# Performance work log

Hardware: AMD Instinct MI355X
Metric: run time of the kernel (lower is better)

Reference implementation:

```python
import jax, jax.numpy as jnp
import numpy as np

B, T, DIM, H, KV, HD = 1, 2048, 2048, 16, 4, 128


def _rope_tables(T, hd):
    half = hd // 2
    inv_freq = 1.0 / (10000.0 ** (np.arange(0, half, dtype=np.float32) / half))
    t = np.arange(T, dtype=np.float32)
    freqs = np.outer(t, inv_freq)                # [T, hd/2]
    emb = np.concatenate([freqs, freqs], axis=-1)  # [T, hd]
    return jnp.asarray(np.cos(emb)), jnp.asarray(np.sin(emb))


def setup_inputs() -> dict:
    key = jax.random.key(0)
    kx, kq, kk, kv, ko = jax.random.split(key, 5)
    s = 0.02
    x = jax.random.normal(kx, (B, T, DIM), dtype=jnp.float32)
    wq = jax.random.normal(kq, (H * HD, DIM), dtype=jnp.float32) * s
    wk = jax.random.normal(kk, (KV * HD, DIM), dtype=jnp.float32) * s
    wv = jax.random.normal(kv, (KV * HD, DIM), dtype=jnp.float32) * s
    wo = jax.random.normal(ko, (DIM, H * HD), dtype=jnp.float32) * s
    cos, sin = _rope_tables(T, HD)
    return {"x": x, "wq": wq, "wk": wk, "wv": wv, "wo": wo, "cos": cos, "sin": sin}


def _rotate_half(u):
    u1, u2 = jnp.split(u, 2, axis=-1)
    return jnp.concatenate([-u2, u1], axis=-1)


def _apply_rope(u, cos, sin):
    # u: [B, T, h, hd]; cos/sin: [T, hd]
    c = cos[None, :, None, :]
    s = sin[None, :, None, :]
    return u * c + _rotate_half(u) * s


def reference(x, wq, wk, wv, wo, cos, sin):
    b, t, dim = x.shape
    hd = cos.shape[1]
    h = wq.shape[0] // hd
    kvh = wk.shape[0] // hd
    rep = h // kvh
    scale = hd ** -0.5

    q = (x @ wq.T).reshape(b, t, h, hd)
    k = (x @ wk.T).reshape(b, t, kvh, hd)
    v = (x @ wv.T).reshape(b, t, kvh, hd)

    q = _apply_rope(q, cos, sin)
    k = _apply_rope(k, cos, sin)

    # Group queries by shared KV head instead of materializing repeat_kv
    qg = q.reshape(b, t, kvh, rep, hd)
    scores = jnp.einsum('bqgrd,bkgd->bgrqk', qg, k) * scale  # [b,g,r,T,T]
    causal = jnp.tril(jnp.ones((t, t), dtype=bool))
    scores = jnp.where(causal[None, None, None], scores, jnp.float32(-1e30))
    attn = jax.nn.softmax(scores, axis=-1)
    out = jnp.einsum('bgrqk,bkgd->bqgrd', attn, v).reshape(b, t, h * hd)
    return out @ wo.T
```

## Files before the change

### kernel.cpp

```cpp
#include <hip/hip_runtime.h>
#include <hip/hip_bf16.h>

typedef unsigned short u16;
typedef __attribute__((ext_vector_type(8))) short bf16x8;
typedef __attribute__((ext_vector_type(4))) float f32x4;

#define T_SEQ 2048
#define DIM   2048
#define NH    16
#define NKV   4
#define HD    128
#define NQKV  3072
#define SCALE 0.08838834764831845f
#define CHUNK 512

__device__ __forceinline__ u16 f2bf(float f) {
  unsigned int u = __float_as_uint(f);
  unsigned int r = (u + 0x7fffu + ((u >> 16) & 1u)) >> 16;
  return (u16)r;
}
__device__ __forceinline__ float bf2f(u16 v) {
  return __uint_as_float(((unsigned int)v) << 16);
}

#define B1 1048576
#define B2 2097152
#define B3 2359296
#define B4 2621440
#define B5 3670016
__global__ void cast_all(const float4* __restrict__ x,  const float4* __restrict__ wq,
                         const float4* __restrict__ wk, const float4* __restrict__ wv,
                         const float4* __restrict__ wo,
                         ushort4* __restrict__ xb, ushort4* __restrict__ wqkvb,
                         ushort4* __restrict__ wob) {
  int i = blockIdx.x * 256 + threadIdx.x;
  const float4* src; ushort4* dst; int j;
  if (i < B1)      { src = x;  dst = xb;               j = i; }
  else if (i < B2) { src = wq; dst = wqkvb;            j = i - B1; }
  else if (i < B3) { src = wk; dst = wqkvb + 1048576;  j = i - B2; }
  else if (i < B4) { src = wv; dst = wqkvb + 1310720;  j = i - B3; }
  else             { src = wo; dst = wob;              j = i - B4; }
  float4 v = src[j];
  ushort4 o;
  o.x = f2bf(v.x); o.y = f2bf(v.y); o.z = f2bf(v.z); o.w = f2bf(v.w);
  dst[j] = o;
}

#define BM 128
#define BN 128
#define BK 64
#define LDP 72

__global__ __launch_bounds__(256) void gemm_bt(
    const u16* __restrict__ A, const u16* __restrict__ W,
    float* __restrict__ Cf, u16* __restrict__ Cb, int M, int N, int K)
{
  __shared__ u16 As[BM * LDP];
  __shared__ u16 Bs[BN * LDP];
  const int tid  = threadIdx.x;
  const int lane = tid & 63;
  const int wave = tid >> 6;
  const int ln   = lane & 15;
  const int quad = lane >> 4;
  const int m0 = blockIdx.y * BM;
  const int n0 = blockIdx.x * BN;
  const int wm = (wave >> 1) * 64;
  const int wn = (wave & 1) * 64;

  const int sr = tid >> 3;
  const int sc = (tid & 7) * 8;

  f32x4 acc[4][4] = {};

  for (int k0 = 0; k0 < K; k0 += BK) {
#pragma unroll
    for (int c = 0; c < 4; ++c) {
      int row = c * 32 + sr;
      *(bf16x8*)&As[row * LDP + sc] =
          *(const bf16x8*)&A[(size_t)(m0 + row) * K + k0 + sc];
      *(bf16x8*)&Bs[row * LDP + sc] =
          *(const bf16x8*)&W[(size_t)(n0 + row) * K + k0 + sc];
    }
    __syncthreads();
#pragma unroll
    for (int ks = 0; ks < 2; ++ks) {
      bf16x8 af[4], bfr[4];
#pragma unroll
      for (int mt = 0; mt < 4; ++mt)
        af[mt] = *(const bf16x8*)&As[(wm + mt * 16 + ln) * LDP + ks * 32 + quad * 8];
#pragma unroll
      for (int nt = 0; nt < 4; ++nt)
        bfr[nt] = *(const bf16x8*)&Bs[(wn + nt * 16 + ln) * LDP + ks * 32 + quad * 8];
#pragma unroll
      for (int mt = 0; mt < 4; ++mt)
#pragma unroll
        for (int nt = 0; nt < 4; ++nt)
          acc[mt][nt] = __builtin_amdgcn_mfma_f32_16x16x32_bf16(
              af[mt], bfr[nt], acc[mt][nt], 0, 0, 0);
    }
    __syncthreads();
  }

#pragma unroll
  for (int mt = 0; mt < 4; ++mt)
#pragma unroll
    for (int nt = 0; nt < 4; ++nt)
#pragma unroll
      for (int r = 0; r < 4; ++r) {
        int row = m0 + wm + mt * 16 + quad * 4 + r;
        int col = n0 + wn + nt * 16 + ln;
        if (Cb) Cb[(size_t)row * N + col] = f2bf(acc[mt][nt][r]);
        else    Cf[(size_t)row * N + col] = acc[mt][nt][r];
      }
}

__global__ void rope_fused(const u16* __restrict__ QKVb,
                           const float* __restrict__ cosT,
                           const float* __restrict__ sinT,
                           u16* __restrict__ Qs, u16* __restrict__ Kb,
                           u16* __restrict__ Vt)
{
  int b = blockIdx.x, d = threadIdx.x;
  if (b < T_SEQ * NH) {
    int t = b >> 4;
    int h = b & 15;
    const u16* row = QKVb + (size_t)t * NQKV + h * HD;
    float u = bf2f(row[d]);
    float pr = (d < 64) ? -bf2f(row[d + 64]) : bf2f(row[d - 64]);
    float c = cosT[t * HD + d], s = sinT[t * HD + d];
    Qs[(size_t)b * HD + d] = f2bf((u * c + pr * s) * SCALE);
  } else if (b < T_SEQ * (NH + NKV)) {
    int b2 = b - T_SEQ * NH;
    int t = b2 >> 2;
    int g = b2 & 3;
    const u16* row = QKVb + (size_t)t * NQKV + DIM + g * HD;
    float u = bf2f(row[d]);
    float pr = (d < 64) ? -bf2f(row[d + 64]) : bf2f(row[d - 64]);
    float c = cosT[t * HD + d], s = sinT[t * HD + d];
    Kb[((size_t)g * T_SEQ + t) * HD + d] = f2bf(u * c + pr * s);
  } else {
    int b3 = b - T_SEQ * (NH + NKV);
    int idx = b3 * 128 + d;
    int t  = idx & (T_SEQ - 1);
    int dd = (idx >> 11) & (HD - 1);
    int g  = idx >> 18;
    Vt[idx] = QKVb[(size_t)t * NQKV + DIM + NKV * HD + g * HD + dd];
  }
}

#define KSP 136
#define VSP 72
#define PSP 72
__global__ __launch_bounds__(256) void flash_partial(
    const u16* __restrict__ Qs, const u16* __restrict__ Kb,
    const u16* __restrict__ Vt, u16* __restrict__ Opart,
    float* __restrict__ lpart)
{
  const int c  = blockIdx.x;
  const int qi = blockIdx.y;
  const int h  = blockIdx.z;
  const int b  = qi >> 2;
  if (c > b) return;
  const int g  = h >> 2;
  const int q0 = qi << 7;
  const int k0 = c << 9;
  const int kend = min(k0 + CHUNK, q0 + 128);

  __shared__ u16 Ks[64 * KSP];
  __shared__ u16 Vs[HD * VSP];
  __shared__ u16 Ps[4][32 * PSP];

  const int tid  = threadIdx.x;
  const int lane = tid & 63;
  const int w    = tid >> 6;
  const int ln   = lane & 15;
  const int quad = lane >> 4;

  bf16x8 aq[2][4];
#pragma unroll
  for (int mt = 0; mt < 2; ++mt) {
    const u16* qp = Qs + ((size_t)(q0 + w * 32 + mt * 16 + ln) * NH + h) * HD + quad * 8;
#pragma unroll
    for (int ks = 0; ks < 4; ++ks) aq[mt][ks] = *(const bf16x8*)&qp[ks * 32];
  }

  f32x4 o[2][8] = {};
  float rs[2][4] = {};

  const int rb0 = q0 + w * 32 + quad * 4;
  const int rb1 = rb0 + 16;
  const int rmax0 = q0 + w * 32 + 15;
  const int rmax1 = q0 + w * 32 + 31;

  const u16* kbase = Kb + (size_t)g * T_SEQ * HD;

  for (int jb = k0; jb < kend; jb += 64) {
    {
      int r = tid >> 4, cc = (tid & 15) * 8;
#pragma unroll
      for (int i = 0; i < 4; ++i) {
        int row = i * 16 + r;
        *(bf16x8*)&Ks[row * KSP + cc] =
            *(const bf16x8*)&kbase[(size_t)(jb + row) * HD + cc];
      }
    }
    {
      int r = tid >> 3, cc = (tid & 7) * 8;
#pragma unroll
      for (int i = 0; i < 4; ++i) {
        int row = i * 32 + r;
        *(bf16x8*)&Vs[row * VSP + cc] =
            *(const bf16x8*)&Vt[(size_t)(g * HD + row) * T_SEQ + jb + cc];
      }
    }
    __syncthreads();

    if (jb <= rmax1) {
      const bool do0  = (jb <= rmax0);
      const bool diag = (jb >= q0);

#pragma unroll
      for (int nb = 0; nb < 4; ++nb) {
        bf16x8 kf[4];
#pragma unroll
        for (int ks = 0; ks < 4; ++ks)
          kf[ks] = *(const bf16x8*)&Ks[(nb * 16 + ln) * KSP + ks * 32 + quad * 8];
        f32x4 s0 = {}, s1 = {};
#pragma unroll
        for (int ks = 0; ks < 4; ++ks) {
          if (do0) s0 = __builtin_amdgcn_mfma_f32_16x16x32_bf16(aq[0][ks], kf[ks], s0, 0, 0, 0);
          s1 = __builtin_amdgcn_mfma_f32_16x16x32_bf16(aq[1][ks], kf[ks], s1, 0, 0, 0);
        }
        const int j = jb + nb * 16 + ln;
#pragma unroll
        for (int r = 0; r < 4; ++r) {
          if (do0) {
            float p = (!diag || j <= rb0 + r) ? __expf(s0[r]) : 0.f;
            rs[0][r] += p;
            Ps[w][(quad * 4 + r) * PSP + nb * 16 + ln] = f2bf(p);
          }
          float p1 = (!diag || j <= rb1 + r) ? __expf(s1[r]) : 0.f;
          rs[1][r] += p1;
          Ps[w][(16 + quad * 4 + r) * PSP + nb * 16 + ln] = f2bf(p1);
        }
      }

#pragma unroll
      for (int kst = 0; kst < 2; ++kst) {
        bf16x8 ap0, ap1;
        if (do0) ap0 = *(const bf16x8*)&Ps[w][ln * PSP + kst * 32 + quad * 8];
        ap1 = *(const bf16x8*)&Ps[w][(16 + ln) * PSP + kst * 32 + quad * 8];
#pragma unroll
        for (int nb8 = 0; nb8 < 8; ++nb8) {
          bf16x8 bv = *(const bf16x8*)&Vs[(nb8 * 16 + ln) * VSP + kst * 32 + quad * 8];
          if (do0) o[0][nb8] = __builtin_amdgcn_mfma_f32_16x16x32_bf16(ap0, bv, o[0][nb8], 0, 0, 0);
          o[1][nb8] = __builtin_amdgcn_mfma_f32_16x16x32_bf16(ap1, bv, o[1][nb8], 0, 0, 0);
        }
      }
    }
    __syncthreads();
  }

  const int slot = h * 40 + 2 * b * (b + 1) + (qi & 3) * (b + 1) + c;
  u16*   op = Opart + (size_t)slot * (128 * 128);
  float* lp = lpart + (size_t)slot * 128;
#pragma unroll
  for (int mt = 0; mt < 2; ++mt) {
#pragma unroll
    for (int r = 0; r < 4; ++r)
#pragma unroll
      for (int off = 1; off < 16; off <<= 1)
        rs[mt][r] += __shfl_xor(rs[mt][r], off);
    int rowb = w * 32 + mt * 16 + quad * 4;
#pragma unroll
    for (int r = 0; r < 4; ++r) {
#pragma unroll
      for (int nb8 = 0; nb8 < 8; ++nb8)
        op[(rowb + r) * 128 + nb8 * 16 + ln] = f2bf(o[mt][nb8][r]);
      if (ln == 0) lp[rowb + r] = rs[mt][r];
    }
  }
}

__global__ void flash_reduce(const u16* __restrict__ Opart,
                             const float* __restrict__ lpart,
                             u16* __restrict__ AO)
{
  const int h = blockIdx.y;
  const int d = threadIdx.x & 127;
  const int t = blockIdx.x * 2 + (threadIdx.x >> 7);
  const int qi = t >> 7, r = t & 127;
  const int b = qi >> 2;
  const int base = h * 40 + 2 * b * (b + 1) + (qi & 3) * (b + 1);
  float so = 0.f, sl = 0.f;
  for (int cc = 0; cc <= b; ++cc) {
    so += bf2f(Opart[(size_t)(base + cc) * (128 * 128) + r * 128 + d]);
    sl += lpart[(size_t)(base + cc) * 128 + r];
  }
  AO[(size_t)t * DIM + h * HD + d] = f2bf(so / sl);
}

extern "C" void kernel_launch(void* const* d_in, const int* in_sizes, int n_in,
                              void* d_out, int out_size, void* d_ws, size_t ws_size,
                              hipStream_t stream) {
  const float* x    = (const float*)d_in[0];
  const float* wq   = (const float*)d_in[1];
  const float* wk   = (const float*)d_in[2];
  const float* wv   = (const float*)d_in[3];
  const float* wo   = (const float*)d_in[4];
  const float* cosT = (const float*)d_in[5];
  const float* sinT = (const float*)d_in[6];
  float* out = (float*)d_out;

  char* ws = (char*)d_ws;
  const size_t MB = 1024 * 1024;
  u16*   xb    = (u16*)(ws + 0 * MB);
  u16*   wqkvb = (u16*)(ws + 8 * MB);
  u16*   wob   = (u16*)(ws + 20 * MB);
  u16*   QKVb  = (u16*)(ws + 28 * MB);
  u16*   Qs    = (u16*)(ws + 8 * MB);
  u16*   Kb    = (u16*)(ws + 16 * MB);
  u16*   Vt    = (u16*)(ws + 18 * MB);
  u16*   AO    = (u16*)(ws + 0 * MB);
  u16*   Opart = (u16*)(ws + 28 * MB);
  float* lpart = (float*)(ws + 48 * MB);

  cast_all<<<B5 / 256, 256, 0, stream>>>(
      (const float4*)x, (const float4*)wq, (const float4*)wk, (const float4*)wv,
      (const float4*)wo, (ushort4*)xb, (ushort4*)wqkvb, (ushort4*)wob);

  gemm_bt<<<dim3(NQKV / BN, T_SEQ / BM), 256, 0, stream>>>(
      xb, wqkvb, nullptr, QKVb, T_SEQ, NQKV, DIM);

  rope_fused<<<T_SEQ * (NH + NKV) + (NKV * HD * T_SEQ) / 128, HD, 0, stream>>>(
      QKVb, cosT, sinT, Qs, Kb, Vt);

  flash_partial<<<dim3(4, 16, 16), 256, 0, stream>>>(Qs, Kb, Vt, Opart, lpart);
  flash_reduce<<<dim3(T_SEQ / 2, NH), 256, 0, stream>>>(Opart, lpart, AO);

  gemm_bt<<<dim3(DIM / BN, T_SEQ / BM), 256, 0, stream>>>(
      AO, wob, out, nullptr, T_SEQ, DIM, DIM);
}
```

Baseline: 284.6 us.

## Process two query heads per flash block to reuse shared K/V tiles

Each flash_partial block now handles two query heads of the same KV group instead of one, halving the grid's z dimension. K and V tiles loaded into shared memory are reused across both heads, halving global K/V traffic and load/sync overhead per unit of work. The cost is doubled accumulator and Q-fragment registers (o becomes 2x2x8 f32x4) plus a larger P buffer in LDS, which may reduce occupancy or cause spills, and fewer blocks are launched.

```diff
diff --git a/kernel.cpp b/kernel.cpp
--- a/kernel.cpp
+++ b/kernel.cpp
@@ -158,17 +158,18 @@
 {
   const int c  = blockIdx.x;
   const int qi = blockIdx.y;
-  const int h  = blockIdx.z;
+  const int hp = blockIdx.z;
   const int b  = qi >> 2;
   if (c > b) return;
-  const int g  = h >> 2;
+  const int g  = hp >> 1;
+  const int h0 = g * 4 + (hp & 1) * 2;
   const int q0 = qi << 7;
   const int k0 = c << 9;
   const int kend = min(k0 + CHUNK, q0 + 128);
 
   __shared__ u16 Ks[64 * KSP];
   __shared__ u16 Vs[HD * VSP];
-  __shared__ u16 Ps[4][32 * PSP];
+  __shared__ u16 Ps[4][64 * PSP];
 
   const int tid  = threadIdx.x;
   const int lane = tid & 63;
@@ -176,16 +177,18 @@
   const int ln   = lane & 15;
   const int quad = lane >> 4;
 
-  bf16x8 aq[2][4];
-#pragma unroll
-  for (int mt = 0; mt < 2; ++mt) {
-    const u16* qp = Qs + ((size_t)(q0 + w * 32 + mt * 16 + ln) * NH + h) * HD + quad * 8;
-#pragma unroll
-    for (int ks = 0; ks < 4; ++ks) aq[mt][ks] = *(const bf16x8*)&qp[ks * 32];
-  }
-
-  f32x4 o[2][8] = {};
-  float rs[2][4] = {};
+  bf16x8 aq[2][2][4];
+#pragma unroll
+  for (int hh = 0; hh < 2; ++hh)
+#pragma unroll
+    for (int mt = 0; mt < 2; ++mt) {
+      const u16* qp = Qs + ((size_t)(q0 + w * 32 + mt * 16 + ln) * NH + h0 + hh) * HD + quad * 8;
+#pragma unroll
+      for (int ks = 0; ks < 4; ++ks) aq[hh][mt][ks] = *(const bf16x8*)&qp[ks * 32];
+    }
+
+  f32x4 o[2][2][8] = {};
+  float rs[2][2][4] = {};
 
   const int rb0 = q0 + w * 32 + quad * 4;
   const int rb1 = rb0 + 16;
@@ -225,59 +228,72 @@
 #pragma unroll
         for (int ks = 0; ks < 4; ++ks)
           kf[ks] = *(const bf16x8*)&Ks[(nb * 16 + ln) * KSP + ks * 32 + quad * 8];
-        f32x4 s0 = {}, s1 = {};
-#pragma unroll
-        for (int ks = 0; ks < 4; ++ks) {
-          if (do0) s0 = __builtin_amdgcn_mfma_f32_16x16x32_bf16(aq[0][ks], kf[ks], s0, 0, 0, 0);
-          s1 = __builtin_amdgcn_mfma_f32_16x16x32_bf16(aq[1][ks], kf[ks], s1, 0, 0, 0);
+        f32x4 s[2][2] = {};
+#pragma unroll
+        for (int ks = 0; ks < 4; ++ks)
+#pragma unroll
+          for (int hh = 0; hh < 2; ++hh) {
+            if (do0) s[hh][0] = __builtin_amdgcn_mfma_f32_16x16x32_bf16(aq[hh][0][ks], kf[ks], s[hh][0], 0, 0, 0);
+            s[hh][1] = __builtin_amdgcn_mfma_f32_16x16x32_bf16(aq[hh][1][ks], kf[ks], s[hh][1], 0, 0, 0);
+          }
+        const int j = jb + nb * 16 + ln;
+#pragma unroll
+        for (int hh = 0; hh < 2; ++hh)
+#pragma unroll
+          for (int r = 0; r < 4; ++r) {
+            if (do0) {
+              float p = (!diag || j <= rb0 + r) ? __expf(s[hh][0][r]) : 0.f;
+              rs[hh][0][r] += p;
+              Ps[w][(hh * 32 + quad * 4 + r) * PSP + nb * 16 + ln] = f2bf(p);
+            }
+            float p1 = (!diag || j <= rb1 + r) ? __expf(s[hh][1][r]) : 0.f;
+            rs[hh][1][r] += p1;
+            Ps[w][(hh * 32 + 16 + quad * 4 + r) * PSP + nb * 16 + ln] = f2bf(p1);
+          }
+      }
+
+#pragma unroll
+      for (int kst = 0; kst < 2; ++kst) {
+        bf16x8 ap[2][2];
+#pragma unroll
+        for (int hh = 0; hh < 2; ++hh) {
+          if (do0) ap[hh][0] = *(const bf16x8*)&Ps[w][(hh * 32 + ln) * PSP + kst * 32 + quad * 8];
+          ap[hh][1] = *(const bf16x8*)&Ps[w][(hh * 32 + 16 + ln) * PSP + kst * 32 + quad * 8];
         }
-        const int j = jb + nb * 16 + ln;
-#pragma unroll
-        for (int r = 0; r < 4; ++r) {
-          if (do0) {
-            float p = (!diag || j <= rb0 + r) ? __expf(s0[r]) : 0.f;
-            rs[0][r] += p;
-            Ps[w][(quad * 4 + r) * PSP + nb * 16 + ln] = f2bf(p);
-          }
-          float p1 = (!diag || j <= rb1 + r) ? __expf(s1[r]) : 0.f;
-          rs[1][r] += p1;
-          Ps[w][(16 + quad * 4 + r) * PSP + nb * 16 + ln] = f2bf(p1);
-        }
-      }
-
-#pragma unroll
-      for (int kst = 0; kst < 2; ++kst) {
-        bf16x8 ap0, ap1;
-        if (do0) ap0 = *(const bf16x8*)&Ps[w][ln * PSP + kst * 32 + quad * 8];
-        ap1 = *(const bf16x8*)&Ps[w][(16 + ln) * PSP + kst * 32 + quad * 8];
 #pragma unroll
         for (int nb8 = 0; nb8 < 8; ++nb8) {
           bf16x8 bv = *(const bf16x8*)&Vs[(nb8 * 16 + ln) * VSP + kst * 32 + quad * 8];
-          if (do0) o[0][nb8] = __builtin_amdgcn_mfma_f32_16x16x32_bf16(ap0, bv, o[0][nb8], 0, 0, 0);
-          o[1][nb8] = __builtin_amdgcn_mfma_f32_16x16x32_bf16(ap1, bv, o[1][nb8], 0, 0, 0);
+#pragma unroll
+          for (int hh = 0; hh < 2; ++hh) {
+            if (do0) o[hh][0][nb8] = __builtin_amdgcn_mfma_f32_16x16x32_bf16(ap[hh][0], bv, o[hh][0][nb8], 0, 0, 0);
+            o[hh][1][nb8] = __builtin_amdgcn_mfma_f32_16x16x32_bf16(ap[hh][1], bv, o[hh][1][nb8], 0, 0, 0);
+          }
         }
       }
     }
     __syncthreads();
   }
 
-  const int slot = h * 40 + 2 * b * (b + 1) + (qi & 3) * (b + 1) + c;
-  u16*   op = Opart + (size_t)slot * (128 * 128);
-  float* lp = lpart + (size_t)slot * 128;
-#pragma unroll
-  for (int mt = 0; mt < 2; ++mt) {
-#pragma unroll
-    for (int r = 0; r < 4; ++r)
-#pragma unroll
-      for (int off = 1; off < 16; off <<= 1)
-        rs[mt][r] += __shfl_xor(rs[mt][r], off);
-    int rowb = w * 32 + mt * 16 + quad * 4;
-#pragma unroll
-    for (int r = 0; r < 4; ++r) {
-#pragma unroll
-      for (int nb8 = 0; nb8 < 8; ++nb8)
-        op[(rowb + r) * 128 + nb8 * 16 + ln] = f2bf(o[mt][nb8][r]);
-      if (ln == 0) lp[rowb + r] = rs[mt][r];
+#pragma unroll
+  for (int hh = 0; hh < 2; ++hh) {
+    const int slot = (h0 + hh) * 40 + 2 * b * (b + 1) + (qi & 3) * (b + 1) + c;
+    u16*   op = Opart + (size_t)slot * (128 * 128);
+    float* lp = lpart + (size_t)slot * 128;
+#pragma unroll
+    for (int mt = 0; mt < 2; ++mt) {
+#pragma unroll
+      for (int r = 0; r < 4; ++r)
+#pragma unroll
+        for (int off = 1; off < 16; off <<= 1)
+          rs[hh][mt][r] += __shfl_xor(rs[hh][mt][r], off);
+      int rowb = w * 32 + mt * 16 + quad * 4;
+#pragma unroll
+      for (int r = 0; r < 4; ++r) {
+#pragma unroll
+        for (int nb8 = 0; nb8 < 8; ++nb8)
+          op[(rowb + r) * 128 + nb8 * 16 + ln] = f2bf(o[hh][mt][nb8][r]);
+        if (ln == 0) lp[rowb + r] = rs[hh][mt][r];
+      }
     }
   }
 }
@@ -335,7 +351,7 @@
   rope_fused<<<T_SEQ * (NH + NKV) + (NKV * HD * T_SEQ) / 128, HD, 0, stream>>>(
       QKVb, cosT, sinT, Qs, Kb, Vt);
 
-  flash_partial<<<dim3(4, 16, 16), 256, 0, stream>>>(Qs, Kb, Vt, Opart, lpart);
+  flash_partial<<<dim3(4, 16, 8), 256, 0, stream>>>(Qs, Kb, Vt, Opart, lpart);
   flash_reduce<<<dim3(T_SEQ / 2, NH), 256, 0, stream>>>(Opart, lpart, AO);
 
   gemm_bt<<<dim3(DIM / BN, T_SEQ / BM), 256, 0, stream>>>(
```

Result: slower. 332.4 us (+16.8%).
